# Kernel optimization log

Hardware: AMD Instinct MI355X
Metric: run time of the kernel (lower is better)

Reference implementation:

```python
import jax, jax.numpy as jnp
import numpy as np

B, H, W = 4, 64, 64
INPLANES, PLANES, G, K = 608, 152, 19, 3
KK = K * K
EPS = 1e-5


def conv2d(x, w, stride=1, padding=0, dilation=1):
    return jax.lax.conv_general_dilated(
        x, w, (stride, stride), [(padding, padding)] * 2,
        rhs_dilation=(dilation, dilation),
        dimension_numbers=("NCHW", "OIHW", "NCHW"))


def bn(x, g, b, m, v):
    # inference-mode batchnorm (affine with running stats)
    inv = g / jnp.sqrt(v + EPS)
    return x * inv[None, :, None, None] + (b - m * inv)[None, :, None, None]


def deform_conv(x, offset, w, pad=1, dil=1):
    # x: [B,C,H,W], offset: [B, 2*G*KK, H, W] ((dy,dx) pairs per group per tap), w: [Cout,C,K,K]
    Bs, C, Hh, Ww = x.shape
    Cg = C // G
    off = offset.reshape(Bs, G, KK, 2, Hh, Ww)
    ky, kx = jnp.meshgrid(jnp.arange(K), jnp.arange(K), indexing="ij")
    base_y = (jnp.arange(Hh) - pad)[None, None, None, :, None] + (dil * ky.reshape(-1))[None, None, :, None, None]
    base_x = (jnp.arange(Ww) - pad)[None, None, None, None, :] + (dil * kx.reshape(-1))[None, None, :, None, None]
    ys = base_y + off[:, :, :, 0]  # [B,G,KK,H,W]
    xs = base_x + off[:, :, :, 1]
    y0 = jnp.floor(ys)
    x0 = jnp.floor(xs)
    wy = ys - y0
    wx = xs - x0
    y0i = y0.astype(jnp.int32)
    x0i = x0.astype(jnp.int32)
    xf = x.reshape(Bs, G, Cg, Hh * Ww)

    def gather(yi, xi, wgt):
        valid = ((yi >= 0) & (yi < Hh) & (xi >= 0) & (xi < Ww)).astype(x.dtype)
        idx = jnp.clip(yi, 0, Hh - 1) * Ww + jnp.clip(xi, 0, Ww - 1)
        idxf = jnp.broadcast_to(idx.reshape(Bs, G, 1, KK * Hh * Ww), (Bs, G, Cg, KK * Hh * Ww))
        g = jnp.take_along_axis(xf, idxf, axis=3).reshape(Bs, G, Cg, KK, Hh, Ww)
        return g * (wgt * valid)[:, :, None]

    samp = (gather(y0i, x0i, (1 - wy) * (1 - wx))
            + gather(y0i, x0i + 1, (1 - wy) * wx)
            + gather(y0i + 1, x0i, wy * (1 - wx))
            + gather(y0i + 1, x0i + 1, wy * wx))  # [B,G,Cg,KK,H,W]
    wr = w.reshape(w.shape[0], G, Cg, KK)
    return jnp.einsum("bgckhw,ogck->bohw", samp, wr)


def setup_inputs() -> dict:
    key = jax.random.key(0)
    ks = jax.random.split(key, 8)
    d = {}
    d["x"] = jax.random.normal(ks[0], (B, INPLANES, H, W), jnp.float32)
    d["conv1_w"] = jax.random.normal(ks[1], (PLANES, INPLANES, 1, 1), jnp.float32) * 0.05
    d["conv2_w"] = jax.random.normal(ks[2], (2 * G * KK, PLANES, 3, 3), jnp.float32) * 0.01
    d["dconv_w"] = jax.random.normal(ks[3], (PLANES, PLANES, 3, 3), jnp.float32) * 0.05
    d["conv3_w"] = jax.random.normal(ks[4], (4 * PLANES, PLANES, 1, 1), jnp.float32) * 0.05
    for i, (name, c) in enumerate([("bn1", PLANES), ("bn2", PLANES), ("bn3", 4 * PLANES)]):
        k1, k2, k3, k4 = jax.random.split(ks[5 + i], 4)
        d[name + "_g"] = jax.random.uniform(k1, (c,), jnp.float32, 0.5, 1.5)
        d[name + "_b"] = jax.random.normal(k2, (c,), jnp.float32) * 0.1
        d[name + "_m"] = jax.random.normal(k3, (c,), jnp.float32) * 0.1
        d[name + "_v"] = jax.random.uniform(k4, (c,), jnp.float32, 0.5, 1.5)
    return d


def reference(x, conv1_w, conv2_w, dconv_w, conv3_w,
              bn1_g, bn1_b, bn1_m, bn1_v,
              bn2_g, bn2_b, bn2_m, bn2_v,
              bn3_g, bn3_b, bn3_m, bn3_v):
    out = jax.nn.relu(conv2d(x, conv1_w))           # conv1 -> relu (order as in source)
    out = bn(out, bn1_g, bn1_b, bn1_m, bn1_v)       # -> bn1
    offset = conv2d(out, conv2_w, padding=1)         # offset-generating 3x3 conv
    out = deform_conv(out, offset, dconv_w)          # deformable 3x3 conv
    out = bn(jax.nn.relu(out), bn2_g, bn2_b, bn2_m, bn2_v)
    out = bn(conv2d(out, conv3_w), bn3_g, bn3_b, bn3_m, bn3_v)
    return jax.nn.relu(out + x)
```

## Files before the change

### kernel.cpp

```cpp
#include <hip/hip_runtime.h>

#define EPSV 1e-5f

typedef __bf16 bf16_t;
typedef __bf16 bf16x8 __attribute__((ext_vector_type(8)));
typedef float f32x4 __attribute__((ext_vector_type(4)));
typedef float f32x8 __attribute__((ext_vector_type(8)));

__device__ inline bf16x8 bzero8() {
  bf16x8 z;
#pragma unroll
  for (int i = 0; i < 8; i++) z[i] = (bf16_t)0.f;
  return z;
}

__device__ inline f32x4 mfma16(bf16x8 a, bf16x8 b, f32x4 c) {
  return __builtin_amdgcn_mfma_f32_16x16x32_bf16(a, b, c, 0, 0, 0);
}

#define W1E (160 * 608)
#define W2E (384 * 1376)
#define WDE (192 * 1440)
#define W3E (640 * 160)

__global__ __launch_bounds__(256) void prep_weights(
    const float* __restrict__ w1, const float* __restrict__ w2,
    const float* __restrict__ wd, const float* __restrict__ w3,
    bf16_t* __restrict__ w1b, bf16_t* __restrict__ w2b,
    bf16_t* __restrict__ wdb, bf16_t* __restrict__ w3b) {
  int i = blockIdx.x * 256 + threadIdx.x;
  float v = 0.f;
  if (i < W1E) {
    int oc = i / 608, ic = i % 608;
    if (oc < 152) v = w1[oc * 608 + ic];
    w1b[i] = (bf16_t)v;
  } else if (i < W1E + W2E) {
    int j = i - W1E;
    int oc = j / 1376, k = j % 1376;
    if (oc < 342 && k < 1368) {
      int t = k / 152, ic = k % 152;
      v = w2[(oc * 152 + ic) * 9 + t];
    }
    w2b[j] = (bf16_t)v;
  } else if (i < W1E + W2E + WDE) {
    int j = i - W1E - W2E;
    int o = j / 1440, k = j % 1440;
    int t = k / 160, ic = k % 160;
    if (o < 152 && ic < 152) v = wd[(o * 152 + ic) * 9 + t];
    wdb[j] = (bf16_t)v;
  } else if (i < W1E + W2E + WDE + W3E) {
    int j = i - W1E - W2E - WDE;
    int oc = j / 160, ic = j % 160;
    if (oc < 608 && ic < 152) v = w3[oc * 152 + ic];
    w3b[j] = (bf16_t)v;
  }
}

__global__ void prep_bn(const float* g1, const float* b1, const float* m1, const float* v1,
                        const float* g2, const float* b2, const float* m2, const float* v2,
                        const float* g3, const float* b3, const float* m3, const float* v3,
                        float* __restrict__ bnc) {
  int i = threadIdx.x;
  if (i < 152) {
    float inv = g1[i] / sqrtf(v1[i] + EPSV);
    bnc[i] = inv;
    bnc[152 + i] = b1[i] - m1[i] * inv;
    float inv2 = g2[i] / sqrtf(v2[i] + EPSV);
    bnc[304 + i] = inv2;
    bnc[456 + i] = b2[i] - m2[i] * inv2;
  }
  if (i < 608) {
    float inv3 = g3[i] / sqrtf(v3[i] + EPSV);
    bnc[608 + i] = inv3;
    bnc[1216 + i] = b3[i] - m3[i] * inv3;
  }
}

__global__ __launch_bounds__(256) void s1_conv1(const float* __restrict__ x,
                                                const bf16_t* __restrict__ w1b,
                                                const float* __restrict__ bnc,
                                                bf16_t* __restrict__ out1) {
  __shared__ bf16_t t1[32 * 616];
  int tid = threadIdx.x;
  int px0 = blockIdx.x * 32;
  int b = px0 >> 12, sp0 = px0 & 4095;
  for (int task = tid; task < 608 * 8; task += 256) {
    int c = task >> 3, i4 = task & 7;
    f32x4 v = *(const f32x4*)(x + (((size_t)(b * 608 + c)) << 12) + sp0 + i4 * 4);
#pragma unroll
    for (int i = 0; i < 4; i++) t1[(i4 * 4 + i) * 616 + c] = (bf16_t)v[i];
  }
  __syncthreads();
  int wid = tid >> 6, lane = tid & 63, q = lane >> 4, lr = lane & 15;
  int mw = wid & 1, nw = wid >> 1;
  f32x4 acc[5];
#pragma unroll
  for (int n = 0; n < 5; n++) acc[n] = (f32x4){0.f, 0.f, 0.f, 0.f};
  for (int kk = 0; kk < 19; kk++) {
    int k0 = kk * 32 + q * 8;
    bf16x8 a = *(const bf16x8*)(t1 + (mw * 16 + lr) * 616 + k0);
#pragma unroll
    for (int n = 0; n < 5; n++) {
      bf16x8 bf = *(const bf16x8*)(w1b + (nw * 80 + n * 16 + lr) * 608 + k0);
      acc[n] = mfma16(a, bf, acc[n]);
    }
  }
#pragma unroll
  for (int n = 0; n < 5; n++) {
    int oc = nw * 80 + n * 16 + lr;
    if (oc < 152) {
      float inv = bnc[oc], beta = bnc[152 + oc];
#pragma unroll
      for (int i = 0; i < 4; i++) {
        int p = px0 + mw * 16 + q * 4 + i;
        float v = fmaxf(acc[n][i], 0.f) * inv + beta;
        out1[(size_t)p * 152 + oc] = (bf16_t)v;
      }
    }
  }
}

__global__ __launch_bounds__(256, 4) void s2_offs(const bf16_t* __restrict__ out1,
                                                  const bf16_t* __restrict__ w2b,
                                                  float* __restrict__ offs) {
  __shared__ bf16_t t2[3 * 34 * 156];
  int tid = threadIdx.x;
  int nh = blockIdx.x & 1;
  int rest = blockIdx.x >> 1;
  int xh = rest & 1, y = (rest >> 1) & 63, b = rest >> 7;
  const bf16_t* ob = out1 + (((size_t)b) << 12) * 152;
  int x0 = xh * 32 - 1;
  for (int task = tid; task < 3 * 34 * 19; task += 256) {
    int j = task / 646, r = task % 646;
    int xi = r / 19, cb = r % 19;
    int yy = y + j - 1, xx = x0 + xi;
    bf16x8 v = bzero8();
    if (yy >= 0 && yy < 64 && xx >= 0 && xx < 64)
      v = *(const bf16x8*)(ob + (size_t)(yy * 64 + xx) * 152 + cb * 8);
    *(bf16x8*)(t2 + (j * 34 + xi) * 156 + cb * 8) = v;
  }
  __syncthreads();
  int wid = tid >> 6, lane = tid & 63, q = lane >> 4, lr = lane & 15;
  int ncol0 = nh * 192 + wid * 48;
  f32x4 acc[2][3];
#pragma unroll
  for (int m = 0; m < 2; m++)
#pragma unroll
    for (int n = 0; n < 3; n++) acc[m][n] = (f32x4){0.f, 0.f, 0.f, 0.f};
  const bf16_t* wb = w2b + (size_t)(ncol0 + lr) * 1376;
#pragma unroll
  for (int kk = 0; kk < 43; kk++) {
    int k0 = kk * 32 + q * 8;
    bf16x8 bfr[3];
#pragma unroll
    for (int n = 0; n < 3; n++)
      bfr[n] = *(const bf16x8*)(wb + (size_t)(n * 16) * 1376 + k0);
    bf16x8 a[2];
    if (k0 < 1368) {
      int t = k0 / 152, c0 = k0 - t * 152;
      int dy = t / 3, dxp1 = t - dy * 3;
#pragma unroll
      for (int m = 0; m < 2; m++)
        a[m] = *(const bf16x8*)(t2 + (dy * 34 + m * 16 + lr + dxp1) * 156 + c0);
    } else {
      a[0] = bzero8();
      a[1] = bzero8();
    }
#pragma unroll
    for (int n = 0; n < 3; n++)
#pragma unroll
      for (int m = 0; m < 2; m++) acc[m][n] = mfma16(a[m], bfr[n], acc[m][n]);
  }
#pragma unroll
  for (int n = 0; n < 3; n++) {
    int col = ncol0 + n * 16 + lr;
    if (col < 342) {
#pragma unroll
      for (int m = 0; m < 2; m++)
#pragma unroll
        for (int i = 0; i < 4; i++) {
          int p = (b << 12) + y * 64 + xh * 32 + m * 16 + q * 4 + i;
          offs[(size_t)p * 344 + col] = acc[m][n][i];
        }
    }
  }
}

__global__ __launch_bounds__(256, 8) void s3_dconv(const bf16_t* __restrict__ out1,
                                                   const float* __restrict__ offs,
                                                   const bf16_t* __restrict__ wdb,
                                                   float* __restrict__ p3) {
  __shared__ bf16_t abuf[16 * 488];
  int tid = threadIdx.x;
  int bi = blockIdx.x;
  int kc = bi % 3, pt = bi / 3;
  int row0 = pt * 16;
  int bb = row0 >> 12;
  const bf16_t* obase = out1 + (((size_t)bb << 12) * 152);
  if (tid < 64) {
    int t = tid >> 4, r = tid & 15;
    int off = (t < 3) ? t * 160 + 152 : 480;
    *(bf16x8*)(abuf + r * 488 + off) = bzero8();
  }
  int t0 = kc * 3;
  for (int task = tid; task < 912; task += 256) {
    int tl = task / 304;
    int rem = task - tl * 304;
    int r = rem / 19, g = rem - r * 19;
    int t = t0 + tl;
    int ky = t / 3, kx = t - ky * 3;
    int p = row0 + r;
    int y = (p >> 6) & 63, xc = p & 63;
    float2 ov = *(const float2*)(offs + (size_t)p * 344 + g * 18 + t * 2);
    float ys = (float)(y - 1 + ky) + ov.x;
    float xs = (float)(xc - 1 + kx) + ov.y;
    float y0f = floorf(ys), x0f = floorf(xs);
    float wy = ys - y0f, wx = xs - x0f;
    int y0 = (int)y0f, x0 = (int)x0f;
    int y1 = y0 + 1, x1 = x0 + 1;
    int y0c = min(max(y0, 0), 63), x0c = min(max(x0, 0), 63);
    int y1c = min(max(y1, 0), 63), x1c = min(max(x1, 0), 63);
    float vy0 = (y0 == y0c) ? 1.f : 0.f;
    float vy1 = (y1 == y1c) ? 1.f : 0.f;
    float vx0 = (x0 == x0c) ? 1.f : 0.f;
    float vx1 = (x1 == x1c) ? 1.f : 0.f;
    float w00 = (1.f - wy) * (1.f - wx) * vy0 * vx0;
    float w01 = (1.f - wy) * wx * vy0 * vx1;
    float w10 = wy * (1.f - wx) * vy1 * vx0;
    float w11 = wy * wx * vy1 * vx1;
    const bf16_t* bg = obase + g * 8;
    bf16x8 c00 = *(const bf16x8*)(bg + (size_t)(y0c * 64 + x0c) * 152);
    bf16x8 c01 = *(const bf16x8*)(bg + (size_t)(y0c * 64 + x1c) * 152);
    bf16x8 c10 = *(const bf16x8*)(bg + (size_t)(y1c * 64 + x0c) * 152);
    bf16x8 c11 = *(const bf16x8*)(bg + (size_t)(y1c * 64 + x1c) * 152);
    bf16x8 o;
#pragma unroll
    for (int i = 0; i < 8; i++) {
      float f = w00 * (float)c00[i];
      f = fmaf(w01, (float)c01[i], f);
      f = fmaf(w10, (float)c10[i], f);
      f = fmaf(w11, (float)c11[i], f);
      o[i] = (bf16_t)f;
    }
    *(bf16x8*)(abuf + r * 488 + tl * 160 + g * 8) = o;
  }
  __syncthreads();
  int wid = tid >> 6, lane = tid & 63, q = lane >> 4, lr = lane & 15;
  f32x4 acc[3];
#pragma unroll
  for (int n = 0; n < 3; n++) acc[n] = (f32x4){0.f, 0.f, 0.f, 0.f};
  const bf16_t* wb = wdb + (size_t)(wid * 48 + lr) * 1440 + kc * 480;
#pragma unroll
  for (int kk = 0; kk < 15; kk++) {
    int k0 = kk * 32 + q * 8;
    bf16x8 a = *(const bf16x8*)(abuf + lr * 488 + k0);
#pragma unroll
    for (int n = 0; n < 3; n++) {
      bf16x8 bf = *(const bf16x8*)(wb + (size_t)(n * 16) * 1440 + k0);
      acc[n] = mfma16(a, bf, acc[n]);
    }
  }
  float* pp = p3 + ((size_t)kc * 16384 + row0) * 192;
#pragma unroll
  for (int n = 0; n < 3; n++) {
    int col = wid * 48 + n * 16 + lr;
#pragma unroll
    for (int i = 0; i < 4; i++) {
      int rr = q * 4 + i;
      pp[(size_t)rr * 192 + col] = acc[n][i];
    }
  }
}

__global__ __launch_bounds__(256) void s4_conv3(const float* __restrict__ p3,
                                                const bf16_t* __restrict__ w3b,
                                                const float* __restrict__ bnc,
                                                const float* __restrict__ x,
                                                float* __restrict__ out) {
  const size_t PSZ = (size_t)16384 * 192;
  int tid = threadIdx.x;
  int wid = tid >> 6, lane = tid & 63, q = lane >> 4, lr = lane & 15;
  int p0 = blockIdx.x * 16;
  int b = p0 >> 12, sp0 = p0 & 4095;
  const float* pbase = p3 + (size_t)(p0 + lr) * 192;
  f32x4 acc[10];
#pragma unroll
  for (int n = 0; n < 10; n++) acc[n] = (f32x4){0.f, 0.f, 0.f, 0.f};
#pragma unroll
  for (int kk = 0; kk < 5; kk++) {
    int k0 = kk * 32 + q * 8;
    bf16x8 a;
    if (k0 < 152) {
      f32x8 s0 = *(const f32x8*)(pbase + k0);
      f32x8 s1 = *(const f32x8*)(pbase + PSZ + k0);
      f32x8 s2 = *(const f32x8*)(pbase + 2 * PSZ + k0);
#pragma unroll
      for (int i = 0; i < 8; i++) {
        float s = s0[i] + s1[i] + s2[i];
        float v = fmaxf(s, 0.f) * bnc[304 + k0 + i] + bnc[456 + k0 + i];
        a[i] = (bf16_t)v;
      }
    } else {
      a = bzero8();
    }
#pragma unroll
    for (int n = 0; n < 10; n++) {
      bf16x8 bf = *(const bf16x8*)(w3b + (size_t)(wid * 160 + n * 16 + lr) * 160 + k0);
      acc[n] = mfma16(a, bf, acc[n]);
    }
  }
#pragma unroll
  for (int n = 0; n < 10; n++) {
    int oc = wid * 160 + n * 16 + lr;
    if (oc < 608) {
      float inv = bnc[608 + oc], beta = bnc[1216 + oc];
      size_t gi = (((size_t)(b * 608 + oc)) << 12) + sp0 + q * 4;
      f32x4 xr = *(const f32x4*)(x + gi);
      f32x4 o;
#pragma unroll
      for (int i = 0; i < 4; i++) o[i] = fmaxf(acc[n][i] * inv + beta + xr[i], 0.f);
      *(f32x4*)(out + gi) = o;
    }
  }
}

extern "C" void kernel_launch(void* const* d_in, const int* in_sizes, int n_in,
                              void* d_out, int out_size, void* d_ws, size_t ws_size,
                              hipStream_t stream) {
  const float* x = (const float*)d_in[0];
  const float* w1 = (const float*)d_in[1];
  const float* w2 = (const float*)d_in[2];
  const float* wd = (const float*)d_in[3];
  const float* w3 = (const float*)d_in[4];
  const float* g1 = (const float*)d_in[5];
  const float* b1 = (const float*)d_in[6];
  const float* m1 = (const float*)d_in[7];
  const float* v1 = (const float*)d_in[8];
  const float* g2 = (const float*)d_in[9];
  const float* b2 = (const float*)d_in[10];
  const float* m2 = (const float*)d_in[11];
  const float* v2 = (const float*)d_in[12];
  const float* g3 = (const float*)d_in[13];
  const float* b3 = (const float*)d_in[14];
  const float* m3 = (const float*)d_in[15];
  const float* v3 = (const float*)d_in[16];

  char* ws = (char*)d_ws;
  bf16_t* w1b = (bf16_t*)(ws + 0);
  bf16_t* w2b = (bf16_t*)(ws + 194560);
  bf16_t* wdb = (bf16_t*)(ws + 1251328);
  bf16_t* w3b = (bf16_t*)(ws + 1804288);
  float* bnc = (float*)(ws + 2009088);
  bf16_t* out1 = (bf16_t*)(ws + 2016384);
  float* offs = (float*)(ws + 6997120);
  float* p3 = (float*)(ws + 29541504);
  float* out = (float*)d_out;

  prep_weights<<<3924, 256, 0, stream>>>(w1, w2, wd, w3, w1b, w2b, wdb, w3b);
  prep_bn<<<1, 640, 0, stream>>>(g1, b1, m1, v1, g2, b2, m2, v2, g3, b3, m3, v3, bnc);
  s1_conv1<<<512, 256, 0, stream>>>(x, w1b, bnc, out1);
  s2_offs<<<1024, 256, 0, stream>>>(out1, w2b, offs);
  s3_dconv<<<3072, 256, 0, stream>>>(out1, offs, wdb, p3);
  s4_conv3<<<1024, 256, 0, stream>>>(p3, w3b, bnc, x, out);
}
```

Measured before the change: 194.7 us.

## Fuse dconv K-split into one block with double-buffered tap pipeline and bf16 output

The deformable conv kernel no longer splits the 9 taps across three blocks that write fp32 partial sums. Each block now loops over all 9 taps, double-buffering the bilinear-sampled tile in shared memory so the gathers for the next tap overlap the MFMAs of the current one. ReLU plus bn2 are applied in the epilogue and stored as a bf16 activation. This removes the fp32 partial buffer traffic and the three-way reduction in conv3, at the cost of fewer blocks (1024 instead of 3072) and a lower occupancy hint.

```diff
diff --git a/kernel.cpp b/kernel.cpp
--- a/kernel.cpp
+++ b/kernel.cpp
@@ -5,7 +5,6 @@
 typedef __bf16 bf16_t;
 typedef __bf16 bf16x8 __attribute__((ext_vector_type(8)));
 typedef float f32x4 __attribute__((ext_vector_type(4)));
-typedef float f32x8 __attribute__((ext_vector_type(8)));
 
 __device__ inline bf16x8 bzero8() {
   bf16x8 z;
@@ -186,123 +185,153 @@
   }
 }
 
-__global__ __launch_bounds__(256, 8) void s3_dconv(const bf16_t* __restrict__ out1,
+#define NT 168
+
+__device__ __forceinline__ void issue_one(const bf16_t* obase, const float* offs,
+                                          int row0, int t, int r, int g,
+                                          bf16x8 c[4], float w[4]) {
+  int p = row0 + r;
+  int y = (p >> 6) & 63, xc = p & 63;
+  int ky = t / 3, kx = t - ky * 3;
+  float2 ov = *(const float2*)(offs + (size_t)p * 344 + g * 18 + t * 2);
+  float ys = (float)(y - 1 + ky) + ov.x;
+  float xs = (float)(xc - 1 + kx) + ov.y;
+  float y0f = floorf(ys), x0f = floorf(xs);
+  float wy = ys - y0f, wx = xs - x0f;
+  int y0 = (int)y0f, x0 = (int)x0f;
+  int y1 = y0 + 1, x1 = x0 + 1;
+  int y0c = min(max(y0, 0), 63), x0c = min(max(x0, 0), 63);
+  int y1c = min(max(y1, 0), 63), x1c = min(max(x1, 0), 63);
+  float vy0 = (y0 == y0c) ? 1.f : 0.f;
+  float vy1 = (y1 == y1c) ? 1.f : 0.f;
+  float vx0 = (x0 == x0c) ? 1.f : 0.f;
+  float vx1 = (x1 == x1c) ? 1.f : 0.f;
+  w[0] = (1.f - wy) * (1.f - wx) * vy0 * vx0;
+  w[1] = (1.f - wy) * wx * vy0 * vx1;
+  w[2] = wy * (1.f - wx) * vy1 * vx0;
+  w[3] = wy * wx * vy1 * vx1;
+  const bf16_t* bg = obase + g * 8;
+  c[0] = *(const bf16x8*)(bg + (size_t)(y0c * 64 + x0c) * 152);
+  c[1] = *(const bf16x8*)(bg + (size_t)(y0c * 64 + x1c) * 152);
+  c[2] = *(const bf16x8*)(bg + (size_t)(y1c * 64 + x0c) * 152);
+  c[3] = *(const bf16x8*)(bg + (size_t)(y1c * 64 + x1c) * 152);
+}
+
+__device__ __forceinline__ void finish_one(bf16_t* dst, const bf16x8 c[4], const float w[4]) {
+  bf16x8 o;
+#pragma unroll
+  for (int i = 0; i < 8; i++) {
+    float f = w[0] * (float)c[0][i];
+    f = fmaf(w[1], (float)c[1][i], f);
+    f = fmaf(w[2], (float)c[2][i], f);
+    f = fmaf(w[3], (float)c[3][i], f);
+    o[i] = (bf16_t)f;
+  }
+  *(bf16x8*)dst = o;
+}
+
+__global__ __launch_bounds__(256, 4) void s3_dconv(const bf16_t* __restrict__ out1,
                                                    const float* __restrict__ offs,
                                                    const bf16_t* __restrict__ wdb,
-                                                   float* __restrict__ p3) {
-  __shared__ bf16_t abuf[16 * 488];
+                                                   const float* __restrict__ bnc,
+                                                   bf16_t* __restrict__ a2) {
+  __shared__ bf16_t bufA[16 * NT];
+  __shared__ bf16_t bufB[16 * NT];
   int tid = threadIdx.x;
-  int bi = blockIdx.x;
-  int kc = bi % 3, pt = bi / 3;
-  int row0 = pt * 16;
+  int row0 = blockIdx.x * 16;
   int bb = row0 >> 12;
   const bf16_t* obase = out1 + (((size_t)bb << 12) * 152);
-  if (tid < 64) {
-    int t = tid >> 4, r = tid & 15;
-    int off = (t < 3) ? t * 160 + 152 : 480;
-    *(bf16x8*)(abuf + r * 488 + off) = bzero8();
-  }
-  int t0 = kc * 3;
-  for (int task = tid; task < 912; task += 256) {
-    int tl = task / 304;
-    int rem = task - tl * 304;
-    int r = rem / 19, g = rem - r * 19;
-    int t = t0 + tl;
-    int ky = t / 3, kx = t - ky * 3;
-    int p = row0 + r;
-    int y = (p >> 6) & 63, xc = p & 63;
-    float2 ov = *(const float2*)(offs + (size_t)p * 344 + g * 18 + t * 2);
-    float ys = (float)(y - 1 + ky) + ov.x;
-    float xs = (float)(xc - 1 + kx) + ov.y;
-    float y0f = floorf(ys), x0f = floorf(xs);
-    float wy = ys - y0f, wx = xs - x0f;
-    int y0 = (int)y0f, x0 = (int)x0f;
-    int y1 = y0 + 1, x1 = x0 + 1;
-    int y0c = min(max(y0, 0), 63), x0c = min(max(x0, 0), 63);
-    int y1c = min(max(y1, 0), 63), x1c = min(max(x1, 0), 63);
-    float vy0 = (y0 == y0c) ? 1.f : 0.f;
-    float vy1 = (y1 == y1c) ? 1.f : 0.f;
-    float vx0 = (x0 == x0c) ? 1.f : 0.f;
-    float vx1 = (x1 == x1c) ? 1.f : 0.f;
-    float w00 = (1.f - wy) * (1.f - wx) * vy0 * vx0;
-    float w01 = (1.f - wy) * wx * vy0 * vx1;
-    float w10 = wy * (1.f - wx) * vy1 * vx0;
-    float w11 = wy * wx * vy1 * vx1;
-    const bf16_t* bg = obase + g * 8;
-    bf16x8 c00 = *(const bf16x8*)(bg + (size_t)(y0c * 64 + x0c) * 152);
-    bf16x8 c01 = *(const bf16x8*)(bg + (size_t)(y0c * 64 + x1c) * 152);
-    bf16x8 c10 = *(const bf16x8*)(bg + (size_t)(y1c * 64 + x0c) * 152);
-    bf16x8 c11 = *(const bf16x8*)(bg + (size_t)(y1c * 64 + x1c) * 152);
-    bf16x8 o;
-#pragma unroll
-    for (int i = 0; i < 8; i++) {
-      float f = w00 * (float)c00[i];
-      f = fmaf(w01, (float)c01[i], f);
-      f = fmaf(w10, (float)c10[i], f);
-      f = fmaf(w11, (float)c11[i], f);
-      o[i] = (bf16_t)f;
-    }
-    *(bf16x8*)(abuf + r * 488 + tl * 160 + g * 8) = o;
-  }
+  if (tid < 32) {
+    int r = tid >> 1;
+    bf16_t* bp = (tid & 1) ? bufB : bufA;
+    *(bf16x8*)(bp + r * NT + 152) = bzero8();
+  }
+  int wid = tid >> 6, lane = tid & 63, q = lane >> 4, lr = lane & 15;
+  int ra = tid / 19, ga = tid - ra * 19;
+  int tb = tid + 256;
+  int rb = tb / 19, gb = tb - rb * 19;
+  bool two = tid < 48;
+  bf16x8 cA[4], cB[4];
+  float wA[4], wB[4];
+  bf16_t* dA_A = bufA + ra * NT + ga * 8;
+  bf16_t* dA_B = bufB + ra * NT + ga * 8;
+  bf16_t* dB_A = bufA + rb * NT + gb * 8;
+  bf16_t* dB_B = bufB + rb * NT + gb * 8;
+
+  f32x4 acc[3];
+#pragma unroll
+  for (int n = 0; n < 3; n++) acc[n] = (f32x4){0.f, 0.f, 0.f, 0.f};
+  const bf16_t* wb = wdb + (size_t)(wid * 48 + lr) * 1440;
+
+  issue_one(obase, offs, row0, 0, ra, ga, cA, wA);
+  if (two) issue_one(obase, offs, row0, 0, rb, gb, cB, wB);
+  finish_one(dA_A, cA, wA);
+  if (two) finish_one(dB_A, cB, wB);
   __syncthreads();
-  int wid = tid >> 6, lane = tid & 63, q = lane >> 4, lr = lane & 15;
-  f32x4 acc[3];
-#pragma unroll
-  for (int n = 0; n < 3; n++) acc[n] = (f32x4){0.f, 0.f, 0.f, 0.f};
-  const bf16_t* wb = wdb + (size_t)(wid * 48 + lr) * 1440 + kc * 480;
-#pragma unroll
-  for (int kk = 0; kk < 15; kk++) {
-    int k0 = kk * 32 + q * 8;
-    bf16x8 a = *(const bf16x8*)(abuf + lr * 488 + k0);
-#pragma unroll
-    for (int n = 0; n < 3; n++) {
-      bf16x8 bf = *(const bf16x8*)(wb + (size_t)(n * 16) * 1440 + k0);
-      acc[n] = mfma16(a, bf, acc[n]);
-    }
-  }
-  float* pp = p3 + ((size_t)kc * 16384 + row0) * 192;
+
+#define PHASE(T, CUR, NXTA, NXTB)                                           \
+  {                                                                         \
+    if ((T) < 8) {                                                          \
+      issue_one(obase, offs, row0, (T) + 1, ra, ga, cA, wA);                \
+      if (two) issue_one(obase, offs, row0, (T) + 1, rb, gb, cB, wB);       \
+    }                                                                       \
+    _Pragma("unroll") for (int kk = 0; kk < 5; kk++) {                      \
+      int k0 = kk * 32 + q * 8;                                             \
+      bf16x8 a = *(const bf16x8*)(CUR + lr * NT + k0);                      \
+      _Pragma("unroll") for (int n = 0; n < 3; n++) {                       \
+        bf16x8 bf =                                                         \
+            *(const bf16x8*)(wb + (size_t)(n * 16) * 1440 + (T)*160 + k0);  \
+        acc[n] = mfma16(a, bf, acc[n]);                                     \
+      }                                                                     \
+    }                                                                       \
+    if ((T) < 8) {                                                          \
+      finish_one(NXTA, cA, wA);                                             \
+      if (two) finish_one(NXTB, cB, wB);                                    \
+    }                                                                       \
+    __syncthreads();                                                        \
+  }
+
+  PHASE(0, bufA, dA_B, dB_B)
+  PHASE(1, bufB, dA_A, dB_A)
+  PHASE(2, bufA, dA_B, dB_B)
+  PHASE(3, bufB, dA_A, dB_A)
+  PHASE(4, bufA, dA_B, dB_B)
+  PHASE(5, bufB, dA_A, dB_A)
+  PHASE(6, bufA, dA_B, dB_B)
+  PHASE(7, bufB, dA_A, dB_A)
+  PHASE(8, bufA, dA_B, dB_B)
+#undef PHASE
+
 #pragma unroll
   for (int n = 0; n < 3; n++) {
-    int col = wid * 48 + n * 16 + lr;
-#pragma unroll
-    for (int i = 0; i < 4; i++) {
-      int rr = q * 4 + i;
-      pp[(size_t)rr * 192 + col] = acc[n][i];
-    }
-  }
-}
-
-__global__ __launch_bounds__(256) void s4_conv3(const float* __restrict__ p3,
+    int oc = wid * 48 + n * 16 + lr;
+    if (oc < 152) {
+      float inv = bnc[304 + oc], beta = bnc[456 + oc];
+#pragma unroll
+      for (int i = 0; i < 4; i++) {
+        int p = row0 + q * 4 + i;
+        float v = fmaxf(acc[n][i], 0.f) * inv + beta;
+        a2[(size_t)p * 152 + oc] = (bf16_t)v;
+      }
+    }
+  }
+}
+
+__global__ __launch_bounds__(256) void s4_conv3(const bf16_t* __restrict__ a2,
                                                 const bf16_t* __restrict__ w3b,
                                                 const float* __restrict__ bnc,
                                                 const float* __restrict__ x,
                                                 float* __restrict__ out) {
-  const size_t PSZ = (size_t)16384 * 192;
   int tid = threadIdx.x;
   int wid = tid >> 6, lane = tid & 63, q = lane >> 4, lr = lane & 15;
   int p0 = blockIdx.x * 16;
   int b = p0 >> 12, sp0 = p0 & 4095;
-  const float* pbase = p3 + (size_t)(p0 + lr) * 192;
   f32x4 acc[10];
 #pragma unroll
   for (int n = 0; n < 10; n++) acc[n] = (f32x4){0.f, 0.f, 0.f, 0.f};
-#pragma unroll
   for (int kk = 0; kk < 5; kk++) {
     int k0 = kk * 32 + q * 8;
-    bf16x8 a;
-    if (k0 < 152) {
-      f32x8 s0 = *(const f32x8*)(pbase + k0);
-      f32x8 s1 = *(const f32x8*)(pbase + PSZ + k0);
-      f32x8 s2 = *(const f32x8*)(pbase + 2 * PSZ + k0);
-#pragma unroll
-      for (int i = 0; i < 8; i++) {
-        float s = s0[i] + s1[i] + s2[i];
-        float v = fmaxf(s, 0.f) * bnc[304 + k0 + i] + bnc[456 + k0 + i];
-        a[i] = (bf16_t)v;
-      }
-    } else {
-      a = bzero8();
-    }
+    bf16x8 a = (k0 < 152) ? *(const bf16x8*)(a2 + (size_t)(p0 + lr) * 152 + k0) : bzero8();
 #pragma unroll
     for (int n = 0; n < 10; n++) {
       bf16x8 bf = *(const bf16x8*)(w3b + (size_t)(wid * 160 + n * 16 + lr) * 160 + k0);
@@ -353,13 +382,13 @@
   float* bnc = (float*)(ws + 2009088);
   bf16_t* out1 = (bf16_t*)(ws + 2016384);
   float* offs = (float*)(ws + 6997120);
-  float* p3 = (float*)(ws + 29541504);
+  bf16_t* a2 = (bf16_t*)(ws + 29541504);
   float* out = (float*)d_out;
 
   prep_weights<<<3924, 256, 0, stream>>>(w1, w2, wd, w3, w1b, w2b, wdb, w3b);
   prep_bn<<<1, 640, 0, stream>>>(g1, b1, m1, v1, g2, b2, m2, v2, g3, b3, m3, v3, bnc);
   s1_conv1<<<512, 256, 0, stream>>>(x, w1b, bnc, out1);
   s2_offs<<<1024, 256, 0, stream>>>(out1, w2b, offs);
-  s3_dconv<<<3072, 256, 0, stream>>>(out1, offs, wdb, p3);
-  s4_conv3<<<1024, 256, 0, stream>>>(p3, w3b, bnc, x, out);
-}
+  s3_dconv<<<1024, 256, 0, stream>>>(out1, offs, wdb, bnc, a2);
+  s4_conv3<<<1024, 256, 0, stream>>>(a2, w3b, bnc, x, out);
+}
```

New measurement: 174.6 us. 10.3% less time.
